# Optimization experiments

Measured on AMD Instinct MI355X. Metric: run time of the kernel, lower is better.

The kernel has to match this reference:

```python
import jax, jax.numpy as jnp
import numpy as np

B = 64          # number of graphs
N_PER = 512     # nodes per graph (equal counts required by final view)
D = 64          # hidden_channels
R = 4           # channel-attention reduction


def setup_inputs() -> dict:
    key = jax.random.key(0)
    k1, k2, k3, k4, k5 = jax.random.split(key, 5)
    M = B * N_PER
    x = jax.random.normal(k1, (M, D), dtype=jnp.float32)
    batch = jnp.repeat(jnp.arange(B, dtype=jnp.int32), N_PER)  # sorted, equal segments
    # channel_attention mode=1 params (torch Linear: y = x @ W.T + b)
    s1 = 1.0 / np.sqrt(D)
    s2 = 1.0 / np.sqrt(D // R)
    W1 = jax.random.uniform(k2, (D // R, D), jnp.float32, -s1, s1)
    b1 = jax.random.uniform(k3, (D // R,), jnp.float32, -s1, s1)
    W2 = jax.random.uniform(k4, (D, D // R), jnp.float32, -s2, s2)
    b2 = jax.random.uniform(k5, (D,), jnp.float32, -s2, s2)
    return {"x": x, "batch": batch, "W1": W1, "b1": b1, "W2": W2, "b2": b2}


def reference(x, batch, W1, b1, W2, b2):
    M, d = x.shape
    # ---- channel_attention (mode=1, sigmoid gate) ----
    sums = jax.ops.segment_sum(x, batch, num_segments=B)                 # [B, D]
    cnts = jax.ops.segment_sum(jnp.ones((M, 1), x.dtype), batch, num_segments=B)
    gap = sums / cnts                                                    # scatter_mean
    h = jax.nn.leaky_relu(gap @ W1.T + b1, negative_slope=0.01)
    imp = jax.nn.sigmoid(h @ W2.T + b2)                                  # [B, D]
    xg = x * imp[batch]                                                  # repeat_interleave broadcast
    # ---- per-node outer product + triu vectorization ----
    # einsum('ik,kj->kij', x.T, x)[k] = outer(x[k], x[k]); take upper triangle (incl diag)
    iu0, iu1 = jnp.triu_indices(d)                                       # row-major triu order
    triu = xg[:, iu0] * xg[:, iu1]                                       # [M, D(D+1)/2]
    return triu.reshape(B, -1)
```

## Files before the change

kernel.cpp:

```cpp
#include <hip/hip_runtime.h>
#include <math.h>

#define NB_GRAPHS 64
#define NPER 512
#define DCH 64
#define DR 16
#define TRIU4 520

__global__ __launch_bounds__(512) void gap_mlp_kernel(
    const float* __restrict__ x,
    const float* __restrict__ W1, const float* __restrict__ b1,
    const float* __restrict__ W2, const float* __restrict__ b2,
    float* __restrict__ imp)
{
    __shared__ float part[32][64];
    __shared__ float sgap[64];
    __shared__ float sh[16];

    const int b   = blockIdx.x;
    const int tid = threadIdx.x;
    const int c4  = tid & 15;
    const int rg  = tid >> 4;

    const float4* xb = reinterpret_cast<const float4*>(x + (size_t)b * NPER * DCH);
    float4 acc = {0.f, 0.f, 0.f, 0.f};
    #pragma unroll
    for (int k = 0; k < 16; ++k) {
        float4 t = xb[(size_t)(rg + 32 * k) * 16 + c4];
        acc.x += t.x; acc.y += t.y; acc.z += t.z; acc.w += t.w;
    }
    part[rg][c4 * 4 + 0] = acc.x;
    part[rg][c4 * 4 + 1] = acc.y;
    part[rg][c4 * 4 + 2] = acc.z;
    part[rg][c4 * 4 + 3] = acc.w;
    __syncthreads();

    if (tid < 64) {
        float t = 0.f;
        #pragma unroll
        for (int g = 0; g < 32; ++g) t += part[g][tid];
        sgap[tid] = t * (1.0f / 512.0f);
    }
    __syncthreads();

    if (tid < DR) {
        float a = b1[tid];
        #pragma unroll
        for (int k = 0; k < 64; ++k) a += sgap[k] * W1[tid * 64 + k];
        sh[tid] = a >= 0.f ? a : 0.01f * a;
    }
    __syncthreads();

    if (tid < 64) {
        float a = b2[tid];
        #pragma unroll
        for (int j = 0; j < DR; ++j) a += sh[j] * W2[tid * DR + j];
        imp[b * 64 + tid] = 1.0f / (1.0f + expf(-a));
    }
}

__global__ __launch_bounds__(256) void sop_kernel(
    const float* __restrict__ x,
    const float* __restrict__ imp,
    float* __restrict__ out)
{
    __shared__ unsigned int tI[TRIU4];
    __shared__ unsigned int tJ[TRIU4];
    __shared__ float v[4][4][64];

    const int tid  = threadIdx.x;
    const int w    = tid >> 6;
    const int lane = tid & 63;
    const int m0   = blockIdx.x * 16;
    const int b    = m0 >> 9;

    for (int t4 = tid; t4 < TRIU4; t4 += 256) {
        unsigned int pi = 0, pj = 0;
        #pragma unroll
        for (int e = 0; e < 4; ++e) {
            int tt = t4 * 4 + e;
            int ii = 0, rem = tt;
            while (rem >= 64 - ii) { rem -= 64 - ii; ++ii; }
            int jj = ii + rem;
            unsigned int ai = ((((unsigned)ii & 3u) << 4) | ((unsigned)ii >> 2)) << 2;
            unsigned int aj = ((((unsigned)jj & 3u) << 4) | ((unsigned)jj >> 2)) << 2;
            pi |= ai << (8 * e);
            pj |= aj << (8 * e);
        }
        tI[t4] = pi;
        tJ[t4] = pj;
    }

    const float4 xv  = reinterpret_cast<const float4*>(x + (size_t)(m0 + 4 * w) * DCH)[lane];
    const float4 iv4 = reinterpret_cast<const float4*>(imp + ((size_t)b << 6))[lane & 15];
    {
        const int n  = lane >> 4;
        const int cc = lane & 15;
        float* vn = &v[w][n][0];
        vn[0 * 16 + cc] = xv.x * iv4.x;
        vn[1 * 16 + cc] = xv.y * iv4.y;
        vn[2 * 16 + cc] = xv.z * iv4.z;
        vn[3 * 16 + cc] = xv.w * iv4.w;
    }

    __syncthreads();

    unsigned int ti[9], tj[9];
    #pragma unroll
    for (int k = 0; k < 9; ++k) {
        int t4 = k * 64 + lane;
        ti[k] = (t4 < TRIU4) ? tI[t4] : 0u;
        tj[k] = (t4 < TRIU4) ? tJ[t4] : 0u;
    }

    #pragma unroll
    for (int it = 0; it < 4; ++it) {
        const int m = m0 + 4 * w + it;
        const char* vb = reinterpret_cast<const char*>(&v[w][it][0]);
        float4* ob = reinterpret_cast<float4*>(out) + (size_t)m * TRIU4;
        #pragma unroll
        for (int k = 0; k < 9; ++k) {
            if (k < 8 || lane < 8) {
                const unsigned int pi = ti[k], pj = tj[k];
                float4 o;
                o.x = *reinterpret_cast<const float*>(vb + (pi & 255u))
                    * *reinterpret_cast<const float*>(vb + (pj & 255u));
                o.y = *reinterpret_cast<const float*>(vb + ((pi >> 8) & 255u))
                    * *reinterpret_cast<const float*>(vb + ((pj >> 8) & 255u));
                o.z = *reinterpret_cast<const float*>(vb + ((pi >> 16) & 255u))
                    * *reinterpret_cast<const float*>(vb + ((pj >> 16) & 255u));
                o.w = *reinterpret_cast<const float*>(vb + (pi >> 24))
                    * *reinterpret_cast<const float*>(vb + (pj >> 24));
                ob[k * 64 + lane] = o;
            }
        }
    }
}

extern "C" void kernel_launch(void* const* d_in, const int* in_sizes, int n_in,
                              void* d_out, int out_size, void* d_ws, size_t ws_size,
                              hipStream_t stream) {
    const float* x  = (const float*)d_in[0];
    const float* W1 = (const float*)d_in[2];
    const float* b1 = (const float*)d_in[3];
    const float* W2 = (const float*)d_in[4];
    const float* b2 = (const float*)d_in[5];
    float* out = (float*)d_out;
    float* imp = (float*)d_ws;

    gap_mlp_kernel<<<NB_GRAPHS, 512, 0, stream>>>(x, W1, b1, W2, b2, imp);
    sop_kernel<<<(NB_GRAPHS * NPER) / 16, 256, 0, stream>>>(x, imp, out);
}
```

Baseline: 294.3 us.

## Compute triu outer product per row with wavefront readlane broadcasts

Drops the shared-memory index tables and the float4 gather scheme. Each wavefront now handles one node: lane j holds the gated value, and for each row i the value is broadcast with readlane, multiplied, and stored with a masked scalar write at the triu row offset. This removes the LDS table setup, the syncthreads and the LDS gathers. In exchange it issues 64 scalar stores per node, many partly masked and not 16-byte vectorized, on a store-bandwidth-bound output.

```diff
diff --git a/kernel.cpp b/kernel.cpp
--- a/kernel.cpp
+++ b/kernel.cpp
@@ -5,7 +5,8 @@
 #define NPER 512
 #define DCH 64
 #define DR 16
-#define TRIU4 520
+#define TRIU 2080
+
 
 __global__ __launch_bounds__(512) void gap_mlp_kernel(
     const float* __restrict__ x,
@@ -64,76 +65,23 @@
     const float* __restrict__ imp,
     float* __restrict__ out)
 {
-    __shared__ unsigned int tI[TRIU4];
-    __shared__ unsigned int tJ[TRIU4];
-    __shared__ float v[4][4][64];
-
     const int tid  = threadIdx.x;
     const int w    = tid >> 6;
     const int lane = tid & 63;
-    const int m0   = blockIdx.x * 16;
-    const int b    = m0 >> 9;
+    const int m    = blockIdx.x * 4 + w;
+    const int b    = m >> 9;
 
-    for (int t4 = tid; t4 < TRIU4; t4 += 256) {
-        unsigned int pi = 0, pj = 0;
-        #pragma unroll
-        for (int e = 0; e < 4; ++e) {
-            int tt = t4 * 4 + e;
-            int ii = 0, rem = tt;
-            while (rem >= 64 - ii) { rem -= 64 - ii; ++ii; }
-            int jj = ii + rem;
-            unsigned int ai = ((((unsigned)ii & 3u) << 4) | ((unsigned)ii >> 2)) << 2;
-            unsigned int aj = ((((unsigned)jj & 3u) << 4) | ((unsigned)jj >> 2)) << 2;
-            pi |= ai << (8 * e);
-            pj |= aj << (8 * e);
-        }
-        tI[t4] = pi;
-        tJ[t4] = pj;
-    }
+    const float xv = x[(size_t)m * DCH + lane];
+    const float iv = imp[((size_t)b << 6) + lane];
+    const float vg = xv * iv;
 
-    const float4 xv  = reinterpret_cast<const float4*>(x + (size_t)(m0 + 4 * w) * DCH)[lane];
-    const float4 iv4 = reinterpret_cast<const float4*>(imp + ((size_t)b << 6))[lane & 15];
-    {
-        const int n  = lane >> 4;
-        const int cc = lane & 15;
-        float* vn = &v[w][n][0];
-        vn[0 * 16 + cc] = xv.x * iv4.x;
-        vn[1 * 16 + cc] = xv.y * iv4.y;
-        vn[2 * 16 + cc] = xv.z * iv4.z;
-        vn[3 * 16 + cc] = xv.w * iv4.w;
-    }
-
-    __syncthreads();
-
-    unsigned int ti[9], tj[9];
+    float* op = out + (size_t)m * TRIU + lane;
     #pragma unroll
-    for (int k = 0; k < 9; ++k) {
-        int t4 = k * 64 + lane;
-        ti[k] = (t4 < TRIU4) ? tI[t4] : 0u;
-        tj[k] = (t4 < TRIU4) ? tJ[t4] : 0u;
-    }
-
-    #pragma unroll
-    for (int it = 0; it < 4; ++it) {
-        const int m = m0 + 4 * w + it;
-        const char* vb = reinterpret_cast<const char*>(&v[w][it][0]);
-        float4* ob = reinterpret_cast<float4*>(out) + (size_t)m * TRIU4;
-        #pragma unroll
-        for (int k = 0; k < 9; ++k) {
-            if (k < 8 || lane < 8) {
-                const unsigned int pi = ti[k], pj = tj[k];
-                float4 o;
-                o.x = *reinterpret_cast<const float*>(vb + (pi & 255u))
-                    * *reinterpret_cast<const float*>(vb + (pj & 255u));
-                o.y = *reinterpret_cast<const float*>(vb + ((pi >> 8) & 255u))
-                    * *reinterpret_cast<const float*>(vb + ((pj >> 8) & 255u));
-                o.z = *reinterpret_cast<const float*>(vb + ((pi >> 16) & 255u))
-                    * *reinterpret_cast<const float*>(vb + ((pj >> 16) & 255u));
-                o.w = *reinterpret_cast<const float*>(vb + (pi >> 24))
-                    * *reinterpret_cast<const float*>(vb + (pj >> 24));
-                ob[k * 64 + lane] = o;
-            }
-        }
+    for (int i = 0; i < 64; ++i) {
+        const float a = __uint_as_float(
+            __builtin_amdgcn_readlane(__float_as_uint(vg), (unsigned)i));
+        if (lane >= i) *op = a * vg;
+        op += (63 - i);
     }
 }
 
@@ -149,5 +97,5 @@
     float* imp = (float*)d_ws;
 
     gap_mlp_kernel<<<NB_GRAPHS, 512, 0, stream>>>(x, W1, b1, W2, b2, imp);
-    sop_kernel<<<(NB_GRAPHS * NPER) / 16, 256, 0, stream>>>(x, imp, out);
+    sop_kernel<<<(NB_GRAPHS * NPER) / 4, 256, 0, stream>>>(x, imp, out);
 }
```

After: 295.6 us. About the same (+0.5%).
